# Kernel optimization log

Hardware: AMD Instinct MI355X
Metric: run time of the kernel (lower is better)

## Reference

```python
import jax, jax.numpy as jnp
import numpy as np
import math

B, H, L, D = 2, 16, 2048, 64


def setup_inputs() -> dict:
    key = jax.random.key(0)
    kq, kk, kv, km, kb = jax.random.split(key, 5)
    Q = jax.random.normal(kq, (B, H, L, D), dtype=jnp.float32)
    K = jax.random.normal(kk, (B, H, L, D), dtype=jnp.float32)
    V = jax.random.normal(kv, (B, H, L, D), dtype=jnp.float32)
    mask = jax.random.randint(km, (B, 1, L, L), 0, 2, dtype=jnp.int32)
    attn_bias = jax.random.normal(kb, (1, H, L, L), dtype=jnp.float32)
    return {"Q": Q, "K": K, "V": V, "mask": mask, "attn_bias": attn_bias,
            "last_layer_flag": 0}


def reference(Q, K, V, mask, attn_bias, last_layer_flag):
    d_tensor = K.shape[-1]
    # score: [B, H, L, L] = Q @ K^T / sqrt(d)
    score = jnp.einsum("bhqd,bhkd->bhqk", Q, K) / math.sqrt(d_tensor)
    if mask is not None:
        score = jnp.where(mask == 0, jnp.float32(-10000.0), score)
    if attn_bias is not None:
        score = score + attn_bias
    if last_layer_flag:
        return jnp.mean(score, axis=1)  # mean over heads: [B, L, L]
    score = jax.nn.softmax(score, axis=-1)
    out = jnp.einsum("bhqk,bhkd->bhqd", score, V)  # [B, H, L, D]
    return (out, score)
```

## Files before the change

### kernel.cpp

```cpp
#include <hip/hip_runtime.h>
#include <hip/hip_bf16.h>

#define Bb 2
#define Hh 16
#define Ll 2048
#define Dd 64
#define OUT_ELEMS (Bb*Hh*Ll*Dd)
#define NT (Ll/64)

typedef __attribute__((ext_vector_type(8))) short bf16x8;
typedef __attribute__((ext_vector_type(4))) float f32x4;
typedef __attribute__((ext_vector_type(4))) int i32x4;

__device__ __forceinline__ unsigned int pk2(float a, float b) {
    unsigned int r;
    asm("v_cvt_pk_bf16_f32 %0, %1, %2" : "=v"(r) : "v"(a), "v"(b));
    return r;
}

__device__ __forceinline__ int swz(int row, int colByte) {
    return row * 128 + (colByte ^ ((row & 7) << 4));
}

__global__ __launch_bounds__(256)
void attn_fused(const float* __restrict__ Q, const float* __restrict__ K,
                const float* __restrict__ V, const int* __restrict__ M,
                const float* __restrict__ Bi, float* __restrict__ out)
{
    __shared__ char Ks[2][64 * 128];
    __shared__ char VTs[2][64 * 128];
    __shared__ char Ps[64 * 128];

    const int bid = blockIdx.x;
    const int b  = bid & 1;
    const int qt = (bid >> 1) & 31;
    const int h  = bid >> 6;
    const int q0 = qt * 64;

    const int tid  = threadIdx.x;
    const int w    = tid >> 6;
    const int lane = tid & 63;
    const int g    = lane >> 4;
    const int c16  = lane & 15;
    const int qr   = w * 16 + c16;

    const float* Qp = Q  + ((size_t)(b * Hh + h) * Ll + q0) * Dd;
    const float* Kp = K  + (size_t)(b * Hh + h) * Ll * Dd;
    const float* Vp = V  + (size_t)(b * Hh + h) * Ll * Dd;
    float* Op = out + ((size_t)(b * Hh + h) * Ll + q0) * Dd;

    const int*   mrow = M  + (size_t)b * Ll * Ll + ((size_t)q0 + qr) * Ll;
    const float* brow = Bi + (size_t)h * Ll * Ll + ((size_t)q0 + qr) * Ll;
    float*       srow = out + OUT_ELEMS + ((size_t)(b * Hh + h) * Ll + q0 + qr) * Ll;

    bf16x8 qf[2];
    {
        const float* qrow = Qp + qr * Dd;
#pragma unroll
        for (int kk = 0; kk < 2; ++kk) {
            f32x4 a = *(const f32x4*)(qrow + kk * 32 + g * 8);
            f32x4 c = *(const f32x4*)(qrow + kk * 32 + g * 8 + 4);
            union { bf16x8 v; unsigned int u[4]; } cvt;
            cvt.u[0] = pk2(a[0], a[1]); cvt.u[1] = pk2(a[2], a[3]);
            cvt.u[2] = pk2(c[0], c[1]); cvt.u[3] = pk2(c[2], c[3]);
            qf[kk] = cvt.v;
        }
    }

    float4 kreg[4];
    float  vreg[16];
    i32x4  m4[4];
    f32x4  b4[4];
    const int r0 = tid >> 4, d0 = (tid & 15) * 4;

    auto issueK = [&](int k0) {
#pragma unroll
        for (int rep = 0; rep < 4; ++rep)
            kreg[rep] = *(const float4*)(Kp + (size_t)(k0 + r0 + rep * 16) * Dd + d0);
    };
    auto writeK = [&](char* buf) {
#pragma unroll
        for (int rep = 0; rep < 4; ++rep) {
            uint2 u = { pk2(kreg[rep].x, kreg[rep].y), pk2(kreg[rep].z, kreg[rep].w) };
            *(uint2*)(buf + swz(r0 + rep * 16, d0 * 2)) = u;
        }
    };
    auto issueV = [&](int k0) {
#pragma unroll
        for (int r = 0; r < 4; ++r)
#pragma unroll
            for (int i = 0; i < 4; ++i)
                vreg[r * 4 + i] = Vp[(size_t)(k0 + w * 16 + r * 4 + i) * Dd + lane];
    };
    auto writeV = [&](char* buf) {
#pragma unroll
        for (int r = 0; r < 4; ++r) {
            uint2 u = { pk2(vreg[r * 4 + 0], vreg[r * 4 + 1]),
                        pk2(vreg[r * 4 + 2], vreg[r * 4 + 3]) };
            *(uint2*)(buf + swz(lane, (w * 16 + r * 4) * 2)) = u;
        }
    };
    auto issueMB = [&](int k0) {
#pragma unroll
        for (int ct = 0; ct < 4; ++ct) {
            m4[ct] = *(const i32x4*)(mrow + k0 + ct * 16 + g * 4);
            b4[ct] = *(const f32x4*)(brow + k0 + ct * 16 + g * 4);
        }
    };

    auto mfmaST = [&](const char* kbuf, f32x4 (&sacc)[4]) {
        __builtin_amdgcn_s_setprio(1);
#pragma unroll
        for (int kk = 0; kk < 2; ++kk) {
#pragma unroll
            for (int ct = 0; ct < 4; ++ct) {
                bf16x8 af = *(const bf16x8*)(kbuf + swz(ct * 16 + c16, kk * 64 + g * 16));
                sacc[ct] = __builtin_amdgcn_mfma_f32_16x16x32_bf16(af, qf[kk], sacc[ct], 0, 0, 0);
            }
        }
        __builtin_amdgcn_s_setprio(0);
    };

    issueK(0);
    issueMB(0);
    writeK(Ks[0]);
    issueK(64);
    __syncthreads();
    float rsv[4] = {0.f, 0.f, 0.f, 0.f};
    for (int t = 0; t < NT; ++t) {
        f32x4 sacc[4] = {{0,0,0,0},{0,0,0,0},{0,0,0,0},{0,0,0,0}};
        mfmaST(Ks[t & 1], sacc);
#pragma unroll
        for (int ct = 0; ct < 4; ++ct)
#pragma unroll
            for (int r = 0; r < 4; ++r) {
                float s = m4[ct][r] == 0 ? -10000.0f
                                         : fmaf(sacc[ct][r], 0.125f, b4[ct][r]);
                rsv[ct] += __expf(s);
            }
        writeK(Ks[(t + 1) & 1]);
        issueK(((t + 2) & (NT - 1)) * 64);
        issueMB(((t + 1) & (NT - 1)) * 64);
        __syncthreads();
    }
    float rs = (rsv[0] + rsv[1]) + (rsv[2] + rsv[3]);
    rs += __shfl_xor(rs, 16);
    rs += __shfl_xor(rs, 32);
    const float inv = 1.0f / rs;

    issueV(0);
    writeV(VTs[0]);
    issueV(64);
    __syncthreads();

    f32x4 oacc[4] = {{0,0,0,0},{0,0,0,0},{0,0,0,0},{0,0,0,0}};
    for (int t = 0; t < NT; ++t) {
        f32x4 sacc[4] = {{0,0,0,0},{0,0,0,0},{0,0,0,0},{0,0,0,0}};
        mfmaST(Ks[t & 1], sacc);
        const int k0 = t * 64;
#pragma unroll
        for (int ct = 0; ct < 4; ++ct) {
            f32x4 p;
#pragma unroll
            for (int r = 0; r < 4; ++r) {
                float s = m4[ct][r] == 0 ? -10000.0f
                                         : fmaf(sacc[ct][r], 0.125f, b4[ct][r]);
                p[r] = __expf(s) * inv;
            }
            __builtin_nontemporal_store(p, (f32x4*)(srow + k0 + ct * 16 + g * 4));
            uint2 u = { pk2(p[0], p[1]), pk2(p[2], p[3]) };
            *(uint2*)(Ps + swz(qr, ct * 32 + g * 8)) = u;
        }
        __builtin_amdgcn_s_setprio(1);
#pragma unroll
        for (int kk = 0; kk < 2; ++kk) {
            bf16x8 pf = *(const bf16x8*)(Ps + swz(qr, kk * 64 + g * 16));
#pragma unroll
            for (int dt = 0; dt < 4; ++dt) {
                bf16x8 vf = *(const bf16x8*)(VTs[t & 1] + swz(dt * 16 + c16, kk * 64 + g * 16));
                oacc[dt] = __builtin_amdgcn_mfma_f32_16x16x32_bf16(pf, vf, oacc[dt], 0, 0, 0);
            }
        }
        __builtin_amdgcn_s_setprio(0);
        if (t + 1 < NT) {
            writeK(Ks[(t + 1) & 1]);
            writeV(VTs[(t + 1) & 1]);
            issueMB((t + 1) * 64);
        }
        if (t + 2 < NT) {
            issueK((t + 2) * 64);
            issueV((t + 2) * 64);
        }
        __syncthreads();
    }

#pragma unroll
    for (int dt = 0; dt < 4; ++dt)
#pragma unroll
        for (int r = 0; r < 4; ++r)
            Op[(w * 16 + g * 4 + r) * Dd + dt * 16 + c16] = oacc[dt][r];
}

extern "C" void kernel_launch(void* const* d_in, const int* in_sizes, int n_in,
                              void* d_out, int out_size, void* d_ws, size_t ws_size,
                              hipStream_t stream) {
    const float* Q  = (const float*)d_in[0];
    const float* K  = (const float*)d_in[1];
    const float* V  = (const float*)d_in[2];
    const int*   M  = (const int*)d_in[3];
    const float* Bi = (const float*)d_in[4];
    float* out = (float*)d_out;

    dim3 grid(Bb * Hh * (Ll / 64));
    dim3 block(256);
    attn_fused<<<grid, block, 0, stream>>>(Q, K, V, M, Bi, out);
}
```

Before: 478.7 us.

## Split fused attention into split-K rowsum and split-K PV kernels

Replaces the single fused kernel (1024 blocks, each running two full passes over keys) with two kernels. The first computes partial softmax denominators over four key chunks and writes them to workspace. The second sums those partials and computes P and P·V over two key halves, combining the outputs with atomic adds into a zeroed output. This raises block count to improve CU occupancy and shortens each block's serial loop. It adds a memset, an extra launch, atomics and workspace traffic, and the PV loop gains an extra barrier because V is now single-buffered.

```diff
diff --git a/kernel.cpp b/kernel.cpp
--- a/kernel.cpp
+++ b/kernel.cpp
@@ -6,7 +6,7 @@
 #define Ll 2048
 #define Dd 64
 #define OUT_ELEMS (Bb*Hh*Ll*Dd)
-#define NT (Ll/64)
+#define BHL (Bb*Hh*Ll)
 
 typedef __attribute__((ext_vector_type(8))) short bf16x8;
 typedef __attribute__((ext_vector_type(4))) float f32x4;
@@ -23,19 +23,19 @@
 }
 
 __global__ __launch_bounds__(256)
-void attn_fused(const float* __restrict__ Q, const float* __restrict__ K,
-                const float* __restrict__ V, const int* __restrict__ M,
-                const float* __restrict__ Bi, float* __restrict__ out)
+void attn_rowsum(const float* __restrict__ Q, const float* __restrict__ K,
+                 const int* __restrict__ M, const float* __restrict__ Bi,
+                 float* __restrict__ ws)
 {
     __shared__ char Ks[2][64 * 128];
-    __shared__ char VTs[2][64 * 128];
-    __shared__ char Ps[64 * 128];
 
     const int bid = blockIdx.x;
-    const int b  = bid & 1;
-    const int qt = (bid >> 1) & 31;
-    const int h  = bid >> 6;
+    const int ks = bid & 3;
+    const int b  = (bid >> 2) & 1;
+    const int qt = (bid >> 3) & 31;
+    const int h  = bid >> 8;
     const int q0 = qt * 64;
+    const int kbase = ks * 512;
 
     const int tid  = threadIdx.x;
     const int w    = tid >> 6;
@@ -44,14 +44,10 @@
     const int c16  = lane & 15;
     const int qr   = w * 16 + c16;
 
-    const float* Qp = Q  + ((size_t)(b * Hh + h) * Ll + q0) * Dd;
-    const float* Kp = K  + (size_t)(b * Hh + h) * Ll * Dd;
-    const float* Vp = V  + (size_t)(b * Hh + h) * Ll * Dd;
-    float* Op = out + ((size_t)(b * Hh + h) * Ll + q0) * Dd;
-
+    const float* Qp = Q + ((size_t)(b * Hh + h) * Ll + q0) * Dd;
+    const float* Kp = K + (size_t)(b * Hh + h) * Ll * Dd;
     const int*   mrow = M  + (size_t)b * Ll * Ll + ((size_t)q0 + qr) * Ll;
     const float* brow = Bi + (size_t)h * Ll * Ll + ((size_t)q0 + qr) * Ll;
-    float*       srow = out + OUT_ELEMS + ((size_t)(b * Hh + h) * Ll + q0 + qr) * Ll;
 
     bf16x8 qf[2];
     {
@@ -68,6 +64,127 @@
     }
 
     float4 kreg[4];
+    i32x4  m4[4];
+    f32x4  b4[4];
+    const int r0 = tid >> 4, d0 = (tid & 15) * 4;
+
+    auto issueK = [&](int k0) {
+#pragma unroll
+        for (int rep = 0; rep < 4; ++rep)
+            kreg[rep] = *(const float4*)(Kp + (size_t)(k0 + r0 + rep * 16) * Dd + d0);
+    };
+    auto writeK = [&](char* buf) {
+#pragma unroll
+        for (int rep = 0; rep < 4; ++rep) {
+            uint2 u = { pk2(kreg[rep].x, kreg[rep].y), pk2(kreg[rep].z, kreg[rep].w) };
+            *(uint2*)(buf + swz(r0 + rep * 16, d0 * 2)) = u;
+        }
+    };
+    auto issueMB = [&](int k0) {
+#pragma unroll
+        for (int ct = 0; ct < 4; ++ct) {
+            m4[ct] = *(const i32x4*)(mrow + k0 + ct * 16 + g * 4);
+            b4[ct] = *(const f32x4*)(brow + k0 + ct * 16 + g * 4);
+        }
+    };
+
+    issueK(kbase);
+    issueMB(kbase);
+    writeK(Ks[0]);
+    issueK(kbase + 64);
+    __syncthreads();
+
+    float rsv[4] = {0.f, 0.f, 0.f, 0.f};
+    for (int t = 0; t < 8; ++t) {
+        f32x4 sacc[4] = {{0,0,0,0},{0,0,0,0},{0,0,0,0},{0,0,0,0}};
+        __builtin_amdgcn_s_setprio(1);
+#pragma unroll
+        for (int kk = 0; kk < 2; ++kk)
+#pragma unroll
+            for (int ct = 0; ct < 4; ++ct) {
+                bf16x8 af = *(const bf16x8*)(Ks[t & 1] + swz(ct * 16 + c16, kk * 64 + g * 16));
+                sacc[ct] = __builtin_amdgcn_mfma_f32_16x16x32_bf16(af, qf[kk], sacc[ct], 0, 0, 0);
+            }
+        __builtin_amdgcn_s_setprio(0);
+#pragma unroll
+        for (int ct = 0; ct < 4; ++ct)
+#pragma unroll
+            for (int r = 0; r < 4; ++r) {
+                float s = m4[ct][r] == 0 ? -10000.0f
+                                         : fmaf(sacc[ct][r], 0.125f, b4[ct][r]);
+                rsv[ct] += __expf(s);
+            }
+        if (t < 7) {
+            writeK(Ks[(t + 1) & 1]);
+            issueMB(kbase + (t + 1) * 64);
+            if (t < 6) issueK(kbase + (t + 2) * 64);
+        }
+        __syncthreads();
+    }
+    float rs = (rsv[0] + rsv[1]) + (rsv[2] + rsv[3]);
+    rs += __shfl_xor(rs, 16);
+    rs += __shfl_xor(rs, 32);
+    if (g == 0)
+        ws[(size_t)ks * BHL + (size_t)(b * Hh + h) * Ll + q0 + qr] = rs;
+}
+
+__global__ __launch_bounds__(256)
+void attn_pv(const float* __restrict__ Q, const float* __restrict__ K,
+             const float* __restrict__ V, const int* __restrict__ M,
+             const float* __restrict__ Bi, const float* __restrict__ ws,
+             float* __restrict__ out)
+{
+    __shared__ char Ks[2][64 * 128];
+    __shared__ char VTs[64 * 128];
+    __shared__ char Ps[64 * 128];
+
+    const int bid = blockIdx.x;
+    const int ks = bid & 1;
+    const int b  = (bid >> 1) & 1;
+    const int qt = (bid >> 2) & 31;
+    const int h  = bid >> 7;
+    const int q0 = qt * 64;
+    const int kbase = ks * 1024;
+    const int NTB = 16;
+
+    const int tid  = threadIdx.x;
+    const int w    = tid >> 6;
+    const int lane = tid & 63;
+    const int g    = lane >> 4;
+    const int c16  = lane & 15;
+    const int qr   = w * 16 + c16;
+
+    const float* Qp = Q + ((size_t)(b * Hh + h) * Ll + q0) * Dd;
+    const float* Kp = K + (size_t)(b * Hh + h) * Ll * Dd;
+    const float* Vp = V + (size_t)(b * Hh + h) * Ll * Dd;
+    float* Op = out + ((size_t)(b * Hh + h) * Ll + q0) * Dd;
+    const int*   mrow = M  + (size_t)b * Ll * Ll + ((size_t)q0 + qr) * Ll;
+    const float* brow = Bi + (size_t)h * Ll * Ll + ((size_t)q0 + qr) * Ll;
+    float*       srow = out + OUT_ELEMS + ((size_t)(b * Hh + h) * Ll + q0 + qr) * Ll;
+
+    float inv;
+    {
+        size_t idx = (size_t)(b * Hh + h) * Ll + q0 + qr;
+        float s = ws[idx] + ws[(size_t)BHL + idx] + ws[2 * (size_t)BHL + idx]
+                + ws[3 * (size_t)BHL + idx];
+        inv = 1.0f / s;
+    }
+
+    bf16x8 qf[2];
+    {
+        const float* qrow = Qp + qr * Dd;
+#pragma unroll
+        for (int kk = 0; kk < 2; ++kk) {
+            f32x4 a = *(const f32x4*)(qrow + kk * 32 + g * 8);
+            f32x4 c = *(const f32x4*)(qrow + kk * 32 + g * 8 + 4);
+            union { bf16x8 v; unsigned int u[4]; } cvt;
+            cvt.u[0] = pk2(a[0], a[1]); cvt.u[1] = pk2(a[2], a[3]);
+            cvt.u[2] = pk2(c[0], c[1]); cvt.u[3] = pk2(c[2], c[3]);
+            qf[kk] = cvt.v;
+        }
+    }
+
+    float4 kreg[4];
     float  vreg[16];
     i32x4  m4[4];
     f32x4  b4[4];
@@ -92,12 +209,12 @@
             for (int i = 0; i < 4; ++i)
                 vreg[r * 4 + i] = Vp[(size_t)(k0 + w * 16 + r * 4 + i) * Dd + lane];
     };
-    auto writeV = [&](char* buf) {
+    auto writeV = [&]() {
 #pragma unroll
         for (int r = 0; r < 4; ++r) {
             uint2 u = { pk2(vreg[r * 4 + 0], vreg[r * 4 + 1]),
                         pk2(vreg[r * 4 + 2], vreg[r * 4 + 3]) };
-            *(uint2*)(buf + swz(lane, (w * 16 + r * 4) * 2)) = u;
+            *(uint2*)(VTs + swz(lane, (w * 16 + r * 4) * 2)) = u;
         }
     };
     auto issueMB = [&](int k0) {
@@ -108,56 +225,32 @@
         }
     };
 
-    auto mfmaST = [&](const char* kbuf, f32x4 (&sacc)[4]) {
+    issueK(kbase);
+    issueMB(kbase);
+    issueV(kbase);
+    writeK(Ks[0]);
+    issueK(kbase + 64);
+
+    f32x4 oacc[4] = {{0,0,0,0},{0,0,0,0},{0,0,0,0},{0,0,0,0}};
+    for (int t = 0; t < NTB; ++t) {
+        const int k0 = kbase + t * 64;
+        __syncthreads();
+        writeV();
+        if (t + 1 < NTB) {
+            writeK(Ks[(t + 1) & 1]);
+            issueV(k0 + 64);
+            if (t + 2 < NTB) issueK(k0 + 128);
+        }
+        f32x4 sacc[4] = {{0,0,0,0},{0,0,0,0},{0,0,0,0},{0,0,0,0}};
         __builtin_amdgcn_s_setprio(1);
 #pragma unroll
-        for (int kk = 0; kk < 2; ++kk) {
+        for (int kk = 0; kk < 2; ++kk)
 #pragma unroll
             for (int ct = 0; ct < 4; ++ct) {
-                bf16x8 af = *(const bf16x8*)(kbuf + swz(ct * 16 + c16, kk * 64 + g * 16));
+                bf16x8 af = *(const bf16x8*)(Ks[t & 1] + swz(ct * 16 + c16, kk * 64 + g * 16));
                 sacc[ct] = __builtin_amdgcn_mfma_f32_16x16x32_bf16(af, qf[kk], sacc[ct], 0, 0, 0);
             }
-        }
         __builtin_amdgcn_s_setprio(0);
-    };
-
-    issueK(0);
-    issueMB(0);
-    writeK(Ks[0]);
-    issueK(64);
-    __syncthreads();
-    float rsv[4] = {0.f, 0.f, 0.f, 0.f};
-    for (int t = 0; t < NT; ++t) {
-        f32x4 sacc[4] = {{0,0,0,0},{0,0,0,0},{0,0,0,0},{0,0,0,0}};
-        mfmaST(Ks[t & 1], sacc);
-#pragma unroll
-        for (int ct = 0; ct < 4; ++ct)
-#pragma unroll
-            for (int r = 0; r < 4; ++r) {
-                float s = m4[ct][r] == 0 ? -10000.0f
-                                         : fmaf(sacc[ct][r], 0.125f, b4[ct][r]);
-                rsv[ct] += __expf(s);
-            }
-        writeK(Ks[(t + 1) & 1]);
-        issueK(((t + 2) & (NT - 1)) * 64);
-        issueMB(((t + 1) & (NT - 1)) * 64);
-        __syncthreads();
-    }
-    float rs = (rsv[0] + rsv[1]) + (rsv[2] + rsv[3]);
-    rs += __shfl_xor(rs, 16);
-    rs += __shfl_xor(rs, 32);
-    const float inv = 1.0f / rs;
-
-    issueV(0);
-    writeV(VTs[0]);
-    issueV(64);
-    __syncthreads();
-
-    f32x4 oacc[4] = {{0,0,0,0},{0,0,0,0},{0,0,0,0},{0,0,0,0}};
-    for (int t = 0; t < NT; ++t) {
-        f32x4 sacc[4] = {{0,0,0,0},{0,0,0,0},{0,0,0,0},{0,0,0,0}};
-        mfmaST(Ks[t & 1], sacc);
-        const int k0 = t * 64;
 #pragma unroll
         for (int ct = 0; ct < 4; ++ct) {
             f32x4 p;
@@ -171,34 +264,26 @@
             uint2 u = { pk2(p[0], p[1]), pk2(p[2], p[3]) };
             *(uint2*)(Ps + swz(qr, ct * 32 + g * 8)) = u;
         }
+        if (t + 1 < NTB) issueMB(k0 + 64);
+        __syncthreads();
         __builtin_amdgcn_s_setprio(1);
 #pragma unroll
         for (int kk = 0; kk < 2; ++kk) {
             bf16x8 pf = *(const bf16x8*)(Ps + swz(qr, kk * 64 + g * 16));
 #pragma unroll
             for (int dt = 0; dt < 4; ++dt) {
-                bf16x8 vf = *(const bf16x8*)(VTs[t & 1] + swz(dt * 16 + c16, kk * 64 + g * 16));
+                bf16x8 vf = *(const bf16x8*)(VTs + swz(dt * 16 + c16, kk * 64 + g * 16));
                 oacc[dt] = __builtin_amdgcn_mfma_f32_16x16x32_bf16(pf, vf, oacc[dt], 0, 0, 0);
             }
         }
         __builtin_amdgcn_s_setprio(0);
-        if (t + 1 < NT) {
-            writeK(Ks[(t + 1) & 1]);
-            writeV(VTs[(t + 1) & 1]);
-            issueMB((t + 1) * 64);
-        }
-        if (t + 2 < NT) {
-            issueK((t + 2) * 64);
-            issueV((t + 2) * 64);
-        }
-        __syncthreads();
     }
 
 #pragma unroll
     for (int dt = 0; dt < 4; ++dt)
 #pragma unroll
         for (int r = 0; r < 4; ++r)
-            Op[(w * 16 + g * 4 + r) * Dd + dt * 16 + c16] = oacc[dt][r];
+            unsafeAtomicAdd(&Op[(w * 16 + g * 4 + r) * Dd + dt * 16 + c16], oacc[dt][r]);
 }
 
 extern "C" void kernel_launch(void* const* d_in, const int* in_sizes, int n_in,
@@ -210,8 +295,10 @@
     const int*   M  = (const int*)d_in[3];
     const float* Bi = (const float*)d_in[4];
     float* out = (float*)d_out;
-
-    dim3 grid(Bb * Hh * (Ll / 64));
-    dim3 block(256);
-    attn_fused<<<grid, block, 0, stream>>>(Q, K, V, M, Bi, out);
-}
+    float* ws  = (float*)d_ws;
+
+    hipMemsetAsync(out, 0, (size_t)OUT_ELEMS * sizeof(float), stream);
+
+    attn_rowsum<<<dim3(4096), dim3(256), 0, stream>>>(Q, K, M, Bi, ws);
+    attn_pv    <<<dim3(2048), dim3(256), 0, stream>>>(Q, K, V, M, Bi, ws, out);
+}
```

New measurement: 511.7 us. 1.07x slower.

## Split attention into exp pass and split-K PV pass with bf16 workspace

Applied to the files above, without the earlier changes.

The single fused two-pass kernel becomes two kernels, each splitting the key dimension into four chunks so the grid is four times larger. The first kernel computes the unnormalized exponentials once, stores them as bf16 in a workspace and writes per-chunk row sums. The second kernel reads them back to normalize, writes the fp32 probabilities, and accumulates the partial P·V into a zeroed output with atomics. This removes the recomputation of QK^T and the mask/bias re-reads in the second pass and adds parallelism, at the cost of an extra bf16 round trip through memory, a memset and atomic adds. The stored probabilities are now bf16-rounded values rescaled, and nothing is computed at all if the workspace is too small.

```diff
diff --git a/kernel.cpp b/kernel.cpp
--- a/kernel.cpp
+++ b/kernel.cpp
@@ -6,36 +6,47 @@
 #define Ll 2048
 #define Dd 64
 #define OUT_ELEMS (Bb*Hh*Ll*Dd)
+#define BHL (Bb*Hh*Ll)
 #define NT (Ll/64)
 
 typedef __attribute__((ext_vector_type(8))) short bf16x8;
 typedef __attribute__((ext_vector_type(4))) float f32x4;
 typedef __attribute__((ext_vector_type(4))) int i32x4;
+typedef __attribute__((ext_vector_type(2))) unsigned int u32x2;
 
 __device__ __forceinline__ unsigned int pk2(float a, float b) {
     unsigned int r;
     asm("v_cvt_pk_bf16_f32 %0, %1, %2" : "=v"(r) : "v"(a), "v"(b));
     return r;
 }
-
+__device__ __forceinline__ float bf2f(short s) {
+    union { float f; unsigned u; } c;
+    c.u = ((unsigned)(unsigned short)s) << 16;
+    return c.f;
+}
+__device__ __forceinline__ void bar() {
+    asm volatile("s_waitcnt lgkmcnt(0)" ::: "memory");
+    __builtin_amdgcn_s_barrier();
+}
 __device__ __forceinline__ int swz(int row, int colByte) {
     return row * 128 + (colByte ^ ((row & 7) << 4));
 }
 
 __global__ __launch_bounds__(256)
-void attn_fused(const float* __restrict__ Q, const float* __restrict__ K,
-                const float* __restrict__ V, const int* __restrict__ M,
-                const float* __restrict__ Bi, float* __restrict__ out)
+void attn_exp(const float* __restrict__ Q, const float* __restrict__ K,
+              const int* __restrict__ M, const float* __restrict__ Bi,
+              float* __restrict__ ws)
 {
     __shared__ char Ks[2][64 * 128];
-    __shared__ char VTs[2][64 * 128];
     __shared__ char Ps[64 * 128];
 
     const int bid = blockIdx.x;
-    const int b  = bid & 1;
-    const int qt = (bid >> 1) & 31;
-    const int h  = bid >> 6;
+    const int ks = bid & 3;
+    const int b  = (bid >> 2) & 1;
+    const int qt = (bid >> 3) & 31;
+    const int h  = bid >> 8;
     const int q0 = qt * 64;
+    const int kb = ks * 512;
 
     const int tid  = threadIdx.x;
     const int w    = tid >> 6;
@@ -44,14 +55,12 @@
     const int c16  = lane & 15;
     const int qr   = w * 16 + c16;
 
-    const float* Qp = Q  + ((size_t)(b * Hh + h) * Ll + q0) * Dd;
-    const float* Kp = K  + (size_t)(b * Hh + h) * Ll * Dd;
-    const float* Vp = V  + (size_t)(b * Hh + h) * Ll * Dd;
-    float* Op = out + ((size_t)(b * Hh + h) * Ll + q0) * Dd;
-
+    const float* Qp = Q + ((size_t)(b * Hh + h) * Ll + q0) * Dd;
+    const float* Kp = K + (size_t)(b * Hh + h) * Ll * Dd;
     const int*   mrow = M  + (size_t)b * Ll * Ll + ((size_t)q0 + qr) * Ll;
     const float* brow = Bi + (size_t)h * Ll * Ll + ((size_t)q0 + qr) * Ll;
-    float*       srow = out + OUT_ELEMS + ((size_t)(b * Hh + h) * Ll + q0 + qr) * Ll;
+    unsigned short* srow = (unsigned short*)(ws + 4 * (size_t)BHL)
+                         + ((size_t)(b * Hh + h) * Ll + q0 + qr) * (size_t)Ll;
 
     bf16x8 qf[2];
     {
@@ -68,7 +77,6 @@
     }
 
     float4 kreg[4];
-    float  vreg[16];
     i32x4  m4[4];
     f32x4  b4[4];
     const int r0 = tid >> 4, d0 = (tid & 15) * 4;
@@ -81,23 +89,8 @@
     auto writeK = [&](char* buf) {
 #pragma unroll
         for (int rep = 0; rep < 4; ++rep) {
-            uint2 u = { pk2(kreg[rep].x, kreg[rep].y), pk2(kreg[rep].z, kreg[rep].w) };
-            *(uint2*)(buf + swz(r0 + rep * 16, d0 * 2)) = u;
-        }
-    };
-    auto issueV = [&](int k0) {
-#pragma unroll
-        for (int r = 0; r < 4; ++r)
-#pragma unroll
-            for (int i = 0; i < 4; ++i)
-                vreg[r * 4 + i] = Vp[(size_t)(k0 + w * 16 + r * 4 + i) * Dd + lane];
-    };
-    auto writeV = [&](char* buf) {
-#pragma unroll
-        for (int r = 0; r < 4; ++r) {
-            uint2 u = { pk2(vreg[r * 4 + 0], vreg[r * 4 + 1]),
-                        pk2(vreg[r * 4 + 2], vreg[r * 4 + 3]) };
-            *(uint2*)(buf + swz(lane, (w * 16 + r * 4) * 2)) = u;
+            u32x2 u = { pk2(kreg[rep].x, kreg[rep].y), pk2(kreg[rep].z, kreg[rep].w) };
+            *(u32x2*)(buf + swz(r0 + rep * 16, d0 * 2)) = u;
         }
     };
     auto issueMB = [&](int k0) {
@@ -108,97 +101,156 @@
         }
     };
 
-    auto mfmaST = [&](const char* kbuf, f32x4 (&sacc)[4]) {
+    issueK(kb);
+    issueMB(kb);
+    writeK(Ks[0]);
+    issueK(kb + 64);
+    bar();
+
+    float rsv[4] = {0.f, 0.f, 0.f, 0.f};
+    for (int t = 0; t < 8; ++t) {
+        f32x4 sacc[4] = {{0,0,0,0},{0,0,0,0},{0,0,0,0},{0,0,0,0}};
         __builtin_amdgcn_s_setprio(1);
 #pragma unroll
-        for (int kk = 0; kk < 2; ++kk) {
+        for (int kk = 0; kk < 2; ++kk)
 #pragma unroll
             for (int ct = 0; ct < 4; ++ct) {
-                bf16x8 af = *(const bf16x8*)(kbuf + swz(ct * 16 + c16, kk * 64 + g * 16));
+                bf16x8 af = *(const bf16x8*)(Ks[t & 1] + swz(ct * 16 + c16, kk * 64 + g * 16));
                 sacc[ct] = __builtin_amdgcn_mfma_f32_16x16x32_bf16(af, qf[kk], sacc[ct], 0, 0, 0);
             }
-        }
         __builtin_amdgcn_s_setprio(0);
-    };
-
-    issueK(0);
-    issueMB(0);
-    writeK(Ks[0]);
-    issueK(64);
-    __syncthreads();
-    float rsv[4] = {0.f, 0.f, 0.f, 0.f};
-    for (int t = 0; t < NT; ++t) {
-        f32x4 sacc[4] = {{0,0,0,0},{0,0,0,0},{0,0,0,0},{0,0,0,0}};
-        mfmaST(Ks[t & 1], sacc);
-#pragma unroll
-        for (int ct = 0; ct < 4; ++ct)
+#pragma unroll
+        for (int ct = 0; ct < 4; ++ct) {
+            f32x4 e;
 #pragma unroll
             for (int r = 0; r < 4; ++r) {
                 float s = m4[ct][r] == 0 ? -10000.0f
                                          : fmaf(sacc[ct][r], 0.125f, b4[ct][r]);
-                rsv[ct] += __expf(s);
-            }
+                e[r] = __expf(s);
+                rsv[ct] += e[r];
+            }
+            u32x2 u = { pk2(e[0], e[1]), pk2(e[2], e[3]) };
+            *(u32x2*)(Ps + swz(qr, ct * 32 + g * 8)) = u;
+        }
+        const int kc = kb + t * 64;
+#pragma unroll
+        for (int half = 0; half < 2; ++half) {
+            bf16x8 d = *(const bf16x8*)(Ps + swz(qr, half * 64 + g * 16));
+            *(bf16x8*)(srow + kc + half * 32 + g * 8) = d;
+        }
         writeK(Ks[(t + 1) & 1]);
-        issueK(((t + 2) & (NT - 1)) * 64);
-        issueMB(((t + 1) & (NT - 1)) * 64);
-        __syncthreads();
+        issueK(kb + ((t + 2) & 7) * 64);
+        issueMB(kb + ((t + 1) & 7) * 64);
+        bar();
     }
     float rs = (rsv[0] + rsv[1]) + (rsv[2] + rsv[3]);
     rs += __shfl_xor(rs, 16);
     rs += __shfl_xor(rs, 32);
-    const float inv = 1.0f / rs;
-
-    issueV(0);
+    if (g == 0)
+        ws[(size_t)ks * BHL + (size_t)(b * Hh + h) * Ll + q0 + qr] = rs;
+}
+
+__global__ __launch_bounds__(256)
+void attn_pv2(const float* __restrict__ V, const float* __restrict__ ws,
+              float* __restrict__ out)
+{
+    __shared__ char VTs[2][64 * 128];
+
+    const int bid = blockIdx.x;
+    const int ks = bid & 3;
+    const int b  = (bid >> 2) & 1;
+    const int qt = (bid >> 3) & 31;
+    const int h  = bid >> 8;
+    const int q0 = qt * 64;
+    const int kb = ks * 512;
+    const int NTB = 8;
+
+    const int tid  = threadIdx.x;
+    const int w    = tid >> 6;
+    const int lane = tid & 63;
+    const int g    = lane >> 4;
+    const int c16  = lane & 15;
+    const int qr   = w * 16 + c16;
+
+    const float* Vp = V + (size_t)(b * Hh + h) * Ll * Dd;
+    float* Op = out + ((size_t)(b * Hh + h) * Ll + q0) * Dd;
+    float* prow = out + OUT_ELEMS + ((size_t)(b * Hh + h) * Ll + q0 + qr) * (size_t)Ll;
+    const unsigned short* srow = (const unsigned short*)(ws + 4 * (size_t)BHL)
+                               + ((size_t)(b * Hh + h) * Ll + q0 + qr) * (size_t)Ll;
+
+    float inv, invO[4];
+    {
+        size_t idx = (size_t)(b * Hh + h) * Ll + q0 + qr;
+        float s = ws[idx] + ws[(size_t)BHL + idx]
+                + ws[2 * (size_t)BHL + idx] + ws[3 * (size_t)BHL + idx];
+        inv = 1.0f / s;
+#pragma unroll
+        for (int r = 0; r < 4; ++r) invO[r] = __shfl(inv, g * 4 + r);
+    }
+
+    float vreg[16];
+    auto issueV = [&](int k0) {
+#pragma unroll
+        for (int r = 0; r < 4; ++r)
+#pragma unroll
+            for (int i = 0; i < 4; ++i)
+                vreg[r * 4 + i] = Vp[(size_t)(k0 + w * 16 + r * 4 + i) * Dd + lane];
+    };
+    auto writeV = [&](char* buf) {
+#pragma unroll
+        for (int r = 0; r < 4; ++r) {
+            u32x2 u = { pk2(vreg[r * 4 + 0], vreg[r * 4 + 1]),
+                        pk2(vreg[r * 4 + 2], vreg[r * 4 + 3]) };
+            *(u32x2*)(buf + swz(lane, (w * 16 + r * 4) * 2)) = u;
+        }
+    };
+
+    bf16x8 pa[2];
+    auto loadA = [&](int t) {
+        pa[0] = *(const bf16x8*)(srow + kb + t * 64 + g * 8);
+        pa[1] = *(const bf16x8*)(srow + kb + t * 64 + 32 + g * 8);
+    };
+
+    issueV(kb);
+    loadA(0);
     writeV(VTs[0]);
-    issueV(64);
-    __syncthreads();
+    issueV(kb + 64);
+    bar();
 
     f32x4 oacc[4] = {{0,0,0,0},{0,0,0,0},{0,0,0,0},{0,0,0,0}};
-    for (int t = 0; t < NT; ++t) {
-        f32x4 sacc[4] = {{0,0,0,0},{0,0,0,0},{0,0,0,0},{0,0,0,0}};
-        mfmaST(Ks[t & 1], sacc);
-        const int k0 = t * 64;
-#pragma unroll
-        for (int ct = 0; ct < 4; ++ct) {
-            f32x4 p;
-#pragma unroll
-            for (int r = 0; r < 4; ++r) {
-                float s = m4[ct][r] == 0 ? -10000.0f
-                                         : fmaf(sacc[ct][r], 0.125f, b4[ct][r]);
-                p[r] = __expf(s) * inv;
-            }
-            __builtin_nontemporal_store(p, (f32x4*)(srow + k0 + ct * 16 + g * 4));
-            uint2 u = { pk2(p[0], p[1]), pk2(p[2], p[3]) };
-            *(uint2*)(Ps + swz(qr, ct * 32 + g * 8)) = u;
-        }
+    for (int t = 0; t < NTB; ++t) {
         __builtin_amdgcn_s_setprio(1);
 #pragma unroll
-        for (int kk = 0; kk < 2; ++kk) {
-            bf16x8 pf = *(const bf16x8*)(Ps + swz(qr, kk * 64 + g * 16));
+        for (int kk = 0; kk < 2; ++kk)
 #pragma unroll
             for (int dt = 0; dt < 4; ++dt) {
                 bf16x8 vf = *(const bf16x8*)(VTs[t & 1] + swz(dt * 16 + c16, kk * 64 + g * 16));
-                oacc[dt] = __builtin_amdgcn_mfma_f32_16x16x32_bf16(pf, vf, oacc[dt], 0, 0, 0);
-            }
-        }
+                oacc[dt] = __builtin_amdgcn_mfma_f32_16x16x32_bf16(pa[kk], vf, oacc[dt], 0, 0, 0);
+            }
         __builtin_amdgcn_s_setprio(0);
-        if (t + 1 < NT) {
-            writeK(Ks[(t + 1) & 1]);
-            writeV(VTs[(t + 1) & 1]);
-            issueMB((t + 1) * 64);
-        }
-        if (t + 2 < NT) {
-            issueK((t + 2) * 64);
-            issueV((t + 2) * 64);
-        }
-        __syncthreads();
-    }
-
+        const int k0 = kb + t * 64;
+#pragma unroll
+        for (int kk = 0; kk < 2; ++kk) {
+            f32x4 p0, p1;
+#pragma unroll
+            for (int j = 0; j < 4; ++j) {
+                p0[j] = bf2f(pa[kk][j]) * inv;
+                p1[j] = bf2f(pa[kk][4 + j]) * inv;
+            }
+            __builtin_nontemporal_store(p0, (f32x4*)(prow + k0 + kk * 32 + g * 8));
+            __builtin_nontemporal_store(p1, (f32x4*)(prow + k0 + kk * 32 + g * 8 + 4));
+        }
+        loadA((t + 1) & 7);
+        writeV(VTs[(t + 1) & 1]);
+        issueV(kb + ((t + 2) & 7) * 64);
+        bar();
+    }
 #pragma unroll
     for (int dt = 0; dt < 4; ++dt)
 #pragma unroll
         for (int r = 0; r < 4; ++r)
-            Op[(w * 16 + g * 4 + r) * Dd + dt * 16 + c16] = oacc[dt][r];
+            unsafeAtomicAdd(&Op[(w * 16 + g * 4 + r) * Dd + dt * 16 + c16],
+                            oacc[dt][r] * invO[r]);
 }
 
 extern "C" void kernel_launch(void* const* d_in, const int* in_sizes, int n_in,
@@ -210,8 +262,13 @@
     const int*   M  = (const int*)d_in[3];
     const float* Bi = (const float*)d_in[4];
     float* out = (float*)d_out;
-
-    dim3 grid(Bb * Hh * (Ll / 64));
-    dim3 block(256);
-    attn_fused<<<grid, block, 0, stream>>>(Q, K, V, M, Bi, out);
-}
+    float* ws  = (float*)d_ws;
+
+    const size_t need = 4ull * BHL * sizeof(float)
+                      + (size_t)BHL * Ll * sizeof(unsigned short);
+    if (ws_size >= need) {
+        (void)hipMemsetAsync(out, 0, (size_t)OUT_ELEMS * sizeof(float), stream);
+        attn_exp<<<dim3(4096), dim3(256), 0, stream>>>(Q, K, M, Bi, ws);
+        attn_pv2<<<dim3(4096), dim3(256), 0, stream>>>(V, ws, out);
+    }
+}
```

Measured after the change: 449.4 us. 6.1% less time.
